# Optimization experiments

Measured on AMD Instinct MI355X. Metric: run time of the kernel, lower is better.

The kernel has to match this reference:

```python
import jax, jax.numpy as jnp
import numpy as np

N = 500000
V = 50000
GF = 64
OC = 256

def _lin(key, din, dout):
    k1, k2 = jax.random.split(key)
    w = jax.random.normal(k1, (din, dout), dtype=jnp.float32) * 0.02
    b = jax.random.normal(k2, (dout,), dtype=jnp.float32) * 0.02
    return w, b

def setup_inputs() -> dict:
    key = jax.random.key(0)
    ks = jax.random.split(key, 12)
    inp_feat = jax.random.normal(ks[0], (N, 6), dtype=jnp.float32)
    vox2point_idx = jax.random.randint(ks[1], (N,), 0, V, dtype=jnp.int32)
    w1x, b1x = _lin(ks[2], 3, GF)
    w2x, b2x = _lin(ks[3], GF, OC // 8)
    w1r, b1r = _lin(ks[4], 3, GF)
    w2r, b2r = _lin(ks[5], GF, OC // 8)
    wax, bax = _lin(ks[6], OC // 4, OC // 8)
    war, bar = _lin(ks[7], OC // 4, OC // 8)
    wv1, bv1 = _lin(ks[8], OC // 2, OC // 2)
    w3, b3 = _lin(ks[9], OC, OC)
    w4, b4 = _lin(ks[10], OC, OC)
    wv2, bv2 = _lin(ks[11], OC, OC)
    return dict(inp_feat=inp_feat, vox2point_idx=vox2point_idx, num_vox=V,
                w1x=w1x, b1x=b1x, w2x=w2x, b2x=b2x,
                w1r=w1r, b1r=b1r, w2r=w2r, b2r=b2r,
                wax=wax, bax=bax, war=war, bar=bar,
                wv1=wv1, bv1=bv1, w3=w3, b3=b3, w4=w4, b4=b4,
                wv2=wv2, bv2=bv2)

def reference(inp_feat, vox2point_idx, num_vox,
              w1x, b1x, w2x, b2x, w1r, b1r, w2r, b2r,
              wax, bax, war, bar, wv1, bv1, w3, b3, w4, b4, wv2, bv2):
    relu = jax.nn.relu
    xyz = inp_feat[:, :3]
    rgb = inp_feat[:, 3:]
    fx = relu(relu(xyz @ w1x + b1x) @ w2x + b2x)   # [N, 32]
    fr = relu(relu(rgb @ w1r + b1r) @ w2r + b2r)   # [N, 32]
    comb = jnp.concatenate([fx, fr], axis=-1)       # [N, 64]
    pf2 = jnp.concatenate([
        fx, fx * jax.nn.sigmoid(comb @ wax + bax),
        fr, fr * jax.nn.sigmoid(comb @ war + bar)], axis=-1)  # [N, 128]
    # scatter-max to voxels; torch_scatter fills empty segments with 0 and
    # pf2 >= 0 elementwise, so clamp -inf (jax empty fill) to 0 for parity.
    vox = jax.ops.segment_max(pf2, vox2point_idx, num_segments=num_vox)
    vox = jnp.maximum(vox, 0.0)                     # [V, 128]
    vox = relu(vox @ wv1 + bv1)
    pg = vox[vox2point_idx]                          # gather back [N, 128]
    pf3 = jnp.concatenate([pg, pf2], axis=-1)        # [N, 256]
    pf5 = relu(relu(pf3 @ w3 + b3) @ w4 + b4)        # [N, 256]
    vox2 = jax.ops.segment_max(pf5, vox2point_idx, num_segments=num_vox)
    vox2 = jnp.maximum(vox2, 0.0)
    return relu(vox2 @ wv2 + bv2)                    # [V, 256]
```

## Files before the change

kernel.cpp:

```cpp
#include <hip/hip_runtime.h>

#define NPTS 500000
#define NVOX 50000
#define NBLK 196

typedef unsigned short u16;
typedef unsigned int u32;
typedef __attribute__((ext_vector_type(8))) short short8;
typedef __attribute__((ext_vector_type(4))) float floatx4;
typedef __attribute__((ext_vector_type(4))) unsigned int uintx4;
typedef __attribute__((ext_vector_type(2))) unsigned int uintx2;

__device__ __forceinline__ u16 f2bf(float f) {
    u32 u = __float_as_uint(f);
    u = u + 0x7fffu + ((u >> 16) & 1u);
    return (u16)(u >> 16);
}

__global__ void k_wtransform(const float* __restrict__ W, u16* __restrict__ Wf, int K, int N) {
    int t = blockIdx.x * 256 + threadIdx.x;
    if (t >= K * N) return;
    int k = t / N, n = t - k * N;
    int kk = k >> 5, q = (k >> 3) & 3, j = k & 7;
    Wf[((size_t)((kk * 4 + q) * N + n) << 3) + j] = f2bf(W[t]);
}

__global__ void k_wcat(const float* __restrict__ w2x, const float* __restrict__ w2r, u16* __restrict__ wcatf) {
    int t = blockIdx.x * 256 + threadIdx.x;
    if (t >= 128 * 64) return;
    int k = t >> 6, n = t & 63;
    float v;
    if (k < 64) v = (n < 32) ? w2x[k * 32 + n] : 0.f;
    else        v = (n >= 32) ? w2r[(k - 64) * 32 + (n - 32)] : 0.f;
    int kk = k >> 5, q = (k >> 3) & 3, j = k & 7;
    wcatf[((size_t)((kk * 4 + q) * 64 + n) << 3) + j] = f2bf(v);
}

__global__ void k_watt(const float* __restrict__ wax, const float* __restrict__ war, u16* __restrict__ wattf) {
    int t = blockIdx.x * 256 + threadIdx.x;
    if (t >= 64 * 64) return;
    int k = t >> 6, n = t & 63;
    float v = (n < 32) ? wax[k * 32 + n] : war[k * 32 + (n - 32)];
    int kk = k >> 5, q = (k >> 3) & 3, j = k & 7;
    wattf[((size_t)((kk * 4 + q) * 64 + n) << 3) + j] = f2bf(v);
}

__global__ void k_hist(const int* __restrict__ idx, int* __restrict__ hcnt) {
    int i = blockIdx.x * 256 + threadIdx.x;
    if (i < NPTS) atomicAdd(&hcnt[idx[i]], 1);
}

__global__ __launch_bounds__(256) void k_scan1(const int* __restrict__ hcnt, int* __restrict__ bsum) {
    __shared__ int wsum[4];
    int t = threadIdx.x;
    int i = blockIdx.x * 256 + t;
    int c = (i < NVOX) ? hcnt[i] : 0;
    #pragma unroll
    for (int d = 32; d >= 1; d >>= 1) c += __shfl_xor(c, d, 64);
    if ((t & 63) == 0) wsum[t >> 6] = c;
    __syncthreads();
    if (t == 0) bsum[blockIdx.x] = wsum[0] + wsum[1] + wsum[2] + wsum[3];
}

__global__ __launch_bounds__(256) void k_scan2(const int* __restrict__ bsum, int* __restrict__ boff) {
    __shared__ int wsum[4];
    int t = threadIdx.x, lane = t & 63, w = t >> 6;
    int c = (t < NBLK) ? bsum[t] : 0;
    int v = c;
    #pragma unroll
    for (int d = 1; d < 64; d <<= 1) {
        int o = __shfl_up(v, d, 64);
        if (lane >= d) v += o;
    }
    if (lane == 63) wsum[w] = v;
    __syncthreads();
    int wo = 0;
    #pragma unroll
    for (int k = 0; k < 4; k++) if (k < w) wo += wsum[k];
    if (t < NBLK) boff[t] = wo + v - c;
}

__global__ __launch_bounds__(256) void k_scan3(const int* __restrict__ hcnt, const int* __restrict__ boff,
                                               int* __restrict__ cur) {
    __shared__ int wsum[4];
    int t = threadIdx.x, lane = t & 63, w = t >> 6;
    int i = blockIdx.x * 256 + t;
    int c = (i < NVOX) ? hcnt[i] : 0;
    int v = c;
    #pragma unroll
    for (int d = 1; d < 64; d <<= 1) {
        int o = __shfl_up(v, d, 64);
        if (lane >= d) v += o;
    }
    if (lane == 63) wsum[w] = v;
    __syncthreads();
    int wo = 0;
    #pragma unroll
    for (int k = 0; k < 4; k++) if (k < w) wo += wsum[k];
    if (i < NVOX) cur[i] = boff[blockIdx.x] + wo + v - c;
}

__global__ void k_scatter(const int* __restrict__ idx, int* __restrict__ cur,
                          int* __restrict__ sptid, int* __restrict__ svid) {
    int i = blockIdx.x * 256 + threadIdx.x;
    if (i < NPTS) {
        int v = idx[i];
        int pos = atomicAdd(&cur[v], 1);
        sptid[pos] = i;
        svid[pos] = v;
    }
}

__global__ __launch_bounds__(256) void k_pointfeat(
    const float* __restrict__ inp, const int* __restrict__ sptid, const int* __restrict__ svid,
    const float* __restrict__ w1x, const float* __restrict__ b1x,
    const float* __restrict__ w1r, const float* __restrict__ b1r,
    const u16* __restrict__ wcatf, const float* __restrict__ b2x, const float* __restrict__ b2r,
    const u16* __restrict__ wattf, const float* __restrict__ bax, const float* __restrict__ bar,
    u16* __restrict__ pf2s, float* __restrict__ voxmax)
{
    __shared__ u16 hbuf[64 * 136];
    __shared__ u16 cbuf[64 * 72];
    __shared__ float wl[512];
    __shared__ int lvid[64];
    int t = threadIdx.x;
    int i0 = blockIdx.x * 64;
    int mcnt = NPTS - i0; if (mcnt > 64) mcnt = 64;
    for (int s = t; s < 512; s += 256) {
        float v;
        if (s < 192)      v = w1x[s];
        else if (s < 256) v = b1x[s - 192];
        else if (s < 448) v = w1r[s - 256];
        else              v = b1r[s - 448];
        wl[s] = v;
    }
    if (t < 64) lvid[t] = (t < mcnt) ? svid[i0 + t] : -1;
    __syncthreads();
    {
        int m = t >> 2, c = t & 3;
        float x0 = 0, x1 = 0, x2 = 0, r0 = 0, r1 = 0, r2 = 0;
        if (m < mcnt) {
            const float* p = inp + (size_t)sptid[i0 + m] * 6;
            x0 = p[0]; x1 = p[1]; x2 = p[2]; r0 = p[3]; r1 = p[4]; r2 = p[5];
        }
        u16* hb = &hbuf[m * 136 + c * 16];
        #pragma unroll
        for (int jp = 0; jp < 8; jp++) {
            int c0 = c * 16 + 2 * jp, c1 = c0 + 1;
            float hx0 = fmaxf(wl[192 + c0] + x0 * wl[c0] + x1 * wl[64 + c0] + x2 * wl[128 + c0], 0.f);
            float hx1 = fmaxf(wl[192 + c1] + x0 * wl[c1] + x1 * wl[64 + c1] + x2 * wl[128 + c1], 0.f);
            float hr0 = fmaxf(wl[448 + c0] + r0 * wl[256 + c0] + r1 * wl[320 + c0] + r2 * wl[384 + c0], 0.f);
            float hr1 = fmaxf(wl[448 + c1] + r0 * wl[256 + c1] + r1 * wl[320 + c1] + r2 * wl[384 + c1], 0.f);
            *(u32*)(hb + 2 * jp)      = (u32)f2bf(hx0) | ((u32)f2bf(hx1) << 16);
            *(u32*)(hb + 64 + 2 * jp) = (u32)f2bf(hr0) | ((u32)f2bf(hr1) << 16);
        }
    }
    __syncthreads();
    int wave = t >> 6, l = t & 63, q = l >> 4, lm = l & 15;
    int n = wave * 16 + lm;
    floatx4 acc[4];
    #pragma unroll
    for (int a = 0; a < 4; a++) acc[a] = (floatx4){0.f, 0.f, 0.f, 0.f};
    #pragma unroll
    for (int kk = 0; kk < 4; kk++) {
        short8 bfrag = *(const short8*)&wcatf[(size_t)((kk * 4 + q) * 64 + n) << 3];
        #pragma unroll
        for (int tm = 0; tm < 4; tm++) {
            short8 afrag = *(const short8*)&hbuf[(tm * 16 + lm) * 136 + kk * 32 + q * 8];
            acc[tm] = __builtin_amdgcn_mfma_f32_16x16x32_bf16(afrag, bfrag, acc[tm], 0, 0, 0);
        }
    }
    float bv = (n < 32) ? b2x[n] : b2r[n - 32];
    float comb_keep[4][4];
    #pragma unroll
    for (int tm = 0; tm < 4; tm++)
        #pragma unroll
        for (int r = 0; r < 4; r++) {
            float v = fmaxf(acc[tm][r] + bv, 0.f);
            comb_keep[tm][r] = v;
            int m = tm * 16 + q * 4 + r;
            cbuf[m * 72 + n] = f2bf(v);
        }
    __syncthreads();
    floatx4 acc2[4];
    #pragma unroll
    for (int a = 0; a < 4; a++) acc2[a] = (floatx4){0.f, 0.f, 0.f, 0.f};
    #pragma unroll
    for (int kk = 0; kk < 2; kk++) {
        short8 bfrag = *(const short8*)&wattf[(size_t)((kk * 4 + q) * 64 + n) << 3];
        #pragma unroll
        for (int tm = 0; tm < 4; tm++) {
            short8 afrag = *(const short8*)&cbuf[(tm * 16 + lm) * 72 + kk * 32 + q * 8];
            acc2[tm] = __builtin_amdgcn_mfma_f32_16x16x32_bf16(afrag, bfrag, acc2[tm], 0, 0, 0);
        }
    }
    float bv2 = (n < 32) ? bax[n] : bar[n - 32];
    int pp = (n < 32) ? n : 32 + n;
    #pragma unroll
    for (int tm = 0; tm < 4; tm++)
        #pragma unroll
        for (int r = 0; r < 4; r++) {
            float att = acc2[tm][r] + bv2;
            float sg = 1.f / (1.f + __expf(-att));
            float plain = comb_keep[tm][r];
            float gated = plain * sg;
            int m = tm * 16 + q * 4 + r;
            hbuf[m * 136 + pp] = f2bf(plain);
            hbuf[m * 136 + pp + 32] = f2bf(gated);
        }
    __syncthreads();
    {
        int row = t >> 2, seg = t & 3;
        if (row < mcnt) {
            const u16* src = &hbuf[row * 136 + seg * 32];
            u16* dst = pf2s + (size_t)(i0 + row) * 128 + seg * 32;
            *(uintx4*)dst = *(const uintx4*)src;
            *(uintx4*)(dst + 8) = *(const uintx4*)(src + 8);
        }
    }
    {
        int c2 = t & 63;
        int h = t >> 6;
        int r0 = h * 16;
        int r1 = r0 + 16; if (r1 > mcnt) r1 = mcnt;
        u32 mlo = 0, mhi = 0;
        int pvid = -1;
        for (int r = r0; r < r1; r++) {
            int vid = lvid[r];
            if (vid != pvid) {
                if (pvid >= 0) {
                    int* addr = (int*)(voxmax + (size_t)pvid * 128 + 2 * c2);
                    if (mlo) atomicMax(addr, (int)(mlo << 16));
                    if (mhi) atomicMax(addr + 1, (int)(mhi << 16));
                }
                pvid = vid; mlo = 0; mhi = 0;
            }
            u32 u = *(const u32*)&hbuf[r * 136 + 2 * c2];
            u32 lo = u & 0xffffu, hi = u >> 16;
            mlo = lo > mlo ? lo : mlo;
            mhi = hi > mhi ? hi : mhi;
        }
        if (pvid >= 0) {
            int* addr = (int*)(voxmax + (size_t)pvid * 128 + 2 * c2);
            if (mlo) atomicMax(addr, (int)(mlo << 16));
            if (mhi) atomicMax(addr + 1, (int)(mhi << 16));
        }
    }
}

template<int K, int N, bool ABF16, bool OUT_BF16>
__global__ __launch_bounds__(256) void k_gemm_relu(
    const void* __restrict__ Ap, const u16* __restrict__ Wf,
    const float* __restrict__ bias, void* __restrict__ outp, int M)
{
    constexpr int STRIDE = K + 8;
    constexpr int TN = N / 64;
    constexpr int KSTEPS = K / 32;
    constexpr int CW = K / 4;
    __shared__ u16 lds[64 * STRIDE];
    int i0 = blockIdx.x * 64;
    int mcnt = M - i0; if (mcnt > 64) mcnt = 64;
    int t = threadIdx.x;
    {
        int row = t >> 2, cseg = t & 3;
        u16* dst = &lds[row * STRIDE + cseg * CW];
        if (row < mcnt) {
            if (ABF16) {
                const u16* src = (const u16*)Ap + (size_t)(i0 + row) * K + cseg * CW;
                #pragma unroll
                for (int c = 0; c < CW / 8; c++)
                    *(uintx4*)(dst + c * 8) = *(const uintx4*)(src + c * 8);
            } else {
                const float* src = (const float*)Ap + (size_t)(i0 + row) * K + cseg * CW;
                #pragma unroll
                for (int c = 0; c < CW / 8; c++) {
                    float4 v0 = *(const float4*)(src + c * 8);
                    float4 v1 = *(const float4*)(src + c * 8 + 4);
                    short8 rr;
                    rr[0] = f2bf(v0.x); rr[1] = f2bf(v0.y); rr[2] = f2bf(v0.z); rr[3] = f2bf(v0.w);
                    rr[4] = f2bf(v1.x); rr[5] = f2bf(v1.y); rr[6] = f2bf(v1.z); rr[7] = f2bf(v1.w);
                    *(short8*)(dst + c * 8) = rr;
                }
            }
        } else {
            short8 z = {0, 0, 0, 0, 0, 0, 0, 0};
            #pragma unroll
            for (int c = 0; c < CW / 8; c++) *(short8*)(dst + c * 8) = z;
        }
    }
    __syncthreads();
    int wave = t >> 6, l = t & 63;
    int q = l >> 4, lm = l & 15;
    int wn0 = wave * (N / 4);
    floatx4 acc[4][TN];
    #pragma unroll
    for (int a = 0; a < 4; a++)
        #pragma unroll
        for (int b = 0; b < TN; b++) acc[a][b] = (floatx4){0.f, 0.f, 0.f, 0.f};
    #pragma unroll
    for (int kk = 0; kk < KSTEPS; kk++) {
        short8 afrag[4], bfrag[TN];
        #pragma unroll
        for (int tm = 0; tm < 4; tm++)
            afrag[tm] = *(const short8*)&lds[(tm * 16 + lm) * STRIDE + kk * 32 + q * 8];
        #pragma unroll
        for (int tn = 0; tn < TN; tn++)
            bfrag[tn] = *(const short8*)&Wf[(size_t)((kk * 4 + q) * N + wn0 + tn * 16 + lm) * 8];
        #pragma unroll
        for (int tm = 0; tm < 4; tm++)
            #pragma unroll
            for (int tn = 0; tn < TN; tn++)
                acc[tm][tn] = __builtin_amdgcn_mfma_f32_16x16x32_bf16(afrag[tm], bfrag[tn], acc[tm][tn], 0, 0, 0);
    }
    #pragma unroll
    for (int tm = 0; tm < 4; tm++)
        #pragma unroll
        for (int tn = 0; tn < TN; tn++) {
            int n = wn0 + tn * 16 + lm;
            float bv = bias[n];
            #pragma unroll
            for (int r = 0; r < 4; r++) {
                int m = tm * 16 + q * 4 + r;
                if (m < mcnt) {
                    float v = fmaxf(acc[tm][tn][r] + bv, 0.f);
                    if (OUT_BF16) ((u16*)outp)[(size_t)(i0 + m) * N + n] = f2bf(v);
                    else          ((float*)outp)[(size_t)(i0 + m) * N + n] = v;
                }
            }
        }
}

__global__ __launch_bounds__(256) void k_pointmlp(
    const u16* __restrict__ voxf, const u16* __restrict__ pf2s, const int* __restrict__ svid,
    const u16* __restrict__ w3f, const float* __restrict__ b3,
    const u16* __restrict__ w4f, const float* __restrict__ b4,
    float* __restrict__ vox2)
{
    constexpr int STRIDE = 264;
    __shared__ u16 lds[64 * STRIDE];
    __shared__ int lvid[64];
    __shared__ float bl[512];
    int i0 = blockIdx.x * 64;
    int mcnt = NPTS - i0; if (mcnt > 64) mcnt = 64;
    int t = threadIdx.x;
    if (t < 64) lvid[t] = (t < mcnt) ? svid[i0 + t] : -1;
    for (int s = t; s < 512; s += 256) bl[s] = (s < 256) ? b3[s] : b4[s - 256];
    {
        int row = t >> 2, cseg = t & 3;
        u16* dst = &lds[row * STRIDE + cseg * 64];
        if (row < mcnt) {
            const u16* src;
            if (cseg < 2) src = voxf + (size_t)svid[i0 + row] * 128 + cseg * 64;
            else          src = pf2s + (size_t)(i0 + row) * 128 + (cseg - 2) * 64;
            #pragma unroll
            for (int c = 0; c < 8; c++)
                *(uintx4*)(dst + c * 8) = *(const uintx4*)(src + c * 8);
        } else {
            uintx4 z = {0, 0, 0, 0};
            #pragma unroll
            for (int c = 0; c < 8; c++) *(uintx4*)(dst + c * 8) = z;
        }
    }
    __syncthreads();
    int wave = t >> 6, l = t & 63;
    int q = l >> 4, lm = l & 15;
    int wm0 = wave * 64;
    floatx4 acc[4][4];
    #pragma unroll
    for (int a = 0; a < 4; a++)
        #pragma unroll
        for (int b = 0; b < 4; b++) acc[a][b] = (floatx4){0.f, 0.f, 0.f, 0.f};
    #pragma unroll
    for (int kk = 0; kk < 8; kk++) {
        short8 wfrag[4], bfrag[4];
        #pragma unroll
        for (int tm = 0; tm < 4; tm++)
            wfrag[tm] = *(const short8*)&w3f[(size_t)((kk * 4 + q) * 256 + wm0 + tm * 16 + lm) * 8];
        #pragma unroll
        for (int tn = 0; tn < 4; tn++)
            bfrag[tn] = *(const short8*)&lds[(tn * 16 + lm) * STRIDE + kk * 32 + q * 8];
        #pragma unroll
        for (int tm = 0; tm < 4; tm++)
            #pragma unroll
            for (int tn = 0; tn < 4; tn++)
                acc[tm][tn] = __builtin_amdgcn_mfma_f32_16x16x32_bf16(wfrag[tm], bfrag[tn], acc[tm][tn], 0, 0, 0);
    }
    __syncthreads();
    #pragma unroll
    for (int tm = 0; tm < 4; tm++) {
        float4 bq = *(const float4*)&bl[wm0 + tm * 16 + 4 * q];
        #pragma unroll
        for (int tn = 0; tn < 4; tn++) {
            u32 lo = (u32)f2bf(fmaxf(acc[tm][tn][0] + bq.x, 0.f)) | ((u32)f2bf(fmaxf(acc[tm][tn][1] + bq.y, 0.f)) << 16);
            u32 hi = (u32)f2bf(fmaxf(acc[tm][tn][2] + bq.z, 0.f)) | ((u32)f2bf(fmaxf(acc[tm][tn][3] + bq.w, 0.f)) << 16);
            *(uintx2*)&lds[(tn * 16 + lm) * STRIDE + wm0 + tm * 16 + 4 * q] = (uintx2){lo, hi};
        }
    }
    __syncthreads();
    floatx4 acc2[4][4];
    #pragma unroll
    for (int a = 0; a < 4; a++)
        #pragma unroll
        for (int b = 0; b < 4; b++) acc2[a][b] = (floatx4){0.f, 0.f, 0.f, 0.f};
    #pragma unroll
    for (int kk = 0; kk < 8; kk++) {
        short8 wfrag[4], bfrag[4];
        #pragma unroll
        for (int tm = 0; tm < 4; tm++)
            wfrag[tm] = *(const short8*)&w4f[(size_t)((kk * 4 + q) * 256 + wm0 + tm * 16 + lm) * 8];
        #pragma unroll
        for (int tn = 0; tn < 4; tn++)
            bfrag[tn] = *(const short8*)&lds[(tn * 16 + lm) * STRIDE + kk * 32 + q * 8];
        #pragma unroll
        for (int tm = 0; tm < 4; tm++)
            #pragma unroll
            for (int tn = 0; tn < 4; tn++)
                acc2[tm][tn] = __builtin_amdgcn_mfma_f32_16x16x32_bf16(wfrag[tm], bfrag[tn], acc2[tm][tn], 0, 0, 0);
    }
    __syncthreads();
    #pragma unroll
    for (int tm = 0; tm < 4; tm++) {
        float4 bq = *(const float4*)&bl[256 + wm0 + tm * 16 + 4 * q];
        #pragma unroll
        for (int tn = 0; tn < 4; tn++) {
            u32 lo = (u32)f2bf(fmaxf(acc2[tm][tn][0] + bq.x, 0.f)) | ((u32)f2bf(fmaxf(acc2[tm][tn][1] + bq.y, 0.f)) << 16);
            u32 hi = (u32)f2bf(fmaxf(acc2[tm][tn][2] + bq.z, 0.f)) | ((u32)f2bf(fmaxf(acc2[tm][tn][3] + bq.w, 0.f)) << 16);
            *(uintx2*)&lds[(tn * 16 + lm) * STRIDE + wm0 + tm * 16 + 4 * q] = (uintx2){lo, hi};
        }
    }
    __syncthreads();
    {
        int c2 = t & 127;
        int h = t >> 7;
        int r0 = h * 32;
        int r1 = r0 + 32; if (r1 > mcnt) r1 = mcnt;
        u32 mlo = 0, mhi = 0;
        int pvid = -1;
        for (int r = r0; r < r1; r++) {
            int vid = lvid[r];
            if (vid != pvid) {
                if (pvid >= 0) {
                    int* addr = (int*)(vox2 + (size_t)pvid * 256 + 2 * c2);
                    if (mlo) atomicMax(addr, (int)(mlo << 16));
                    if (mhi) atomicMax(addr + 1, (int)(mhi << 16));
                }
                pvid = vid; mlo = 0; mhi = 0;
            }
            u32 u = *(const u32*)&lds[r * STRIDE + 2 * c2];
            u32 lo = u & 0xffffu, hi = u >> 16;
            mlo = lo > mlo ? lo : mlo;
            mhi = hi > mhi ? hi : mhi;
        }
        if (pvid >= 0) {
            int* addr = (int*)(vox2 + (size_t)pvid * 256 + 2 * c2);
            if (mlo) atomicMax(addr, (int)(mlo << 16));
            if (mhi) atomicMax(addr + 1, (int)(mhi << 16));
        }
    }
}

extern "C" void kernel_launch(void* const* d_in, const int* in_sizes, int n_in,
                              void* d_out, int out_size, void* d_ws, size_t ws_size,
                              hipStream_t stream) {
    const float* inp = (const float*)d_in[0];
    const int*   idx = (const int*)d_in[1];
    const float* w1x = (const float*)d_in[3];  const float* b1x = (const float*)d_in[4];
    const float* w2x = (const float*)d_in[5];  const float* b2x = (const float*)d_in[6];
    const float* w1r = (const float*)d_in[7];  const float* b1r = (const float*)d_in[8];
    const float* w2r = (const float*)d_in[9];  const float* b2r = (const float*)d_in[10];
    const float* wax = (const float*)d_in[11]; const float* bax = (const float*)d_in[12];
    const float* war = (const float*)d_in[13]; const float* bar = (const float*)d_in[14];
    const float* wv1 = (const float*)d_in[15]; const float* bv1 = (const float*)d_in[16];
    const float* w3  = (const float*)d_in[17]; const float* b3  = (const float*)d_in[18];
    const float* w4  = (const float*)d_in[19]; const float* b4  = (const float*)d_in[20];
    const float* wv2 = (const float*)d_in[21]; const float* bv2 = (const float*)d_in[22];
    float* out = (float*)d_out;

    char* ws = (char*)d_ws;
    u16*   pf2s   = (u16*)ws;   ws += (size_t)NPTS * 128 * sizeof(u16);
    float* voxmax = (float*)ws; ws += (size_t)NVOX * 128 * sizeof(float);
    u16*   voxf   = (u16*)ws;   ws += (size_t)NVOX * 128 * sizeof(u16);
    float* vox2   = (float*)ws; ws += (size_t)NVOX * 256 * sizeof(float);
    u16*   w3f    = (u16*)ws;   ws += 65536 * sizeof(u16);
    u16*   w4f    = (u16*)ws;   ws += 65536 * sizeof(u16);
    u16*   wv1f   = (u16*)ws;   ws += 16384 * sizeof(u16);
    u16*   wv2f   = (u16*)ws;   ws += 65536 * sizeof(u16);
    u16*   wcatf  = (u16*)ws;   ws += 8192 * sizeof(u16);
    u16*   wattf  = (u16*)ws;   ws += 4096 * sizeof(u16);
    int*   hcnt   = (int*)ws;   ws += (size_t)NVOX * sizeof(int);
    int*   cur    = (int*)ws;   ws += (size_t)NVOX * sizeof(int);
    int*   bsum   = (int*)ws;   ws += (size_t)NBLK * sizeof(int);
    int*   boff   = (int*)ws;   ws += (size_t)NBLK * sizeof(int);
    int*   sptid  = (int*)ws;   ws += (size_t)NPTS * sizeof(int);
    int*   svid   = (int*)ws;   ws += (size_t)NPTS * sizeof(int);

    hipMemsetAsync(hcnt, 0, (size_t)NVOX * sizeof(int), stream);
    hipMemsetAsync(voxmax, 0, (size_t)NVOX * 128 * sizeof(float), stream);
    hipMemsetAsync(vox2, 0, (size_t)NVOX * 256 * sizeof(float), stream);

    k_wtransform<<<256, 256, 0, stream>>>(w3, w3f, 256, 256);
    k_wtransform<<<256, 256, 0, stream>>>(w4, w4f, 256, 256);
    k_wtransform<<<64,  256, 0, stream>>>(wv1, wv1f, 128, 128);
    k_wtransform<<<256, 256, 0, stream>>>(wv2, wv2f, 256, 256);
    k_wcat<<<32, 256, 0, stream>>>(w2x, w2r, wcatf);
    k_watt<<<16, 256, 0, stream>>>(wax, war, wattf);

    k_hist<<<(NPTS + 255) / 256, 256, 0, stream>>>(idx, hcnt);
    k_scan1<<<NBLK, 256, 0, stream>>>(hcnt, bsum);
    k_scan2<<<1, 256, 0, stream>>>(bsum, boff);
    k_scan3<<<NBLK, 256, 0, stream>>>(hcnt, boff, cur);
    k_scatter<<<(NPTS + 255) / 256, 256, 0, stream>>>(idx, cur, sptid, svid);

    k_pointfeat<<<(NPTS + 63) / 64, 256, 0, stream>>>(
        inp, sptid, svid, w1x, b1x, w1r, b1r, wcatf, b2x, b2r, wattf, bax, bar, pf2s, voxmax);

    k_gemm_relu<128, 128, false, true><<<(NVOX + 63) / 64, 256, 0, stream>>>(
        (const void*)voxmax, wv1f, bv1, (void*)voxf, NVOX);

    k_pointmlp<<<(NPTS + 63) / 64, 256, 0, stream>>>(
        voxf, pf2s, svid, w3f, b3, w4f, b4, vox2);

    k_gemm_relu<256, 256, false, false><<<(NVOX + 63) / 64, 256, 0, stream>>>(
        (const void*)vox2, wv2f, bv2, (void*)out, NVOX);
}
```

Baseline: 507.3 us.

## Swizzle pointmlp LDS, prefetch weights, use hardware bf16 pack and packed max

Replaces software bf16 rounding with the v_cvt_pk_bf16_f32 instruction and uses packed u16 max for the segment-max reductions. The pointmlp kernel drops its padded LDS stride for an XOR-swizzled 256-wide layout, which shrinks shared memory and raises the occupancy hint to 4 blocks per CU. It also double-buffers weight fragments across k-steps and reworks the final scatter so each thread handles 4 channels over 16 rows. Several independent micro-optimizations are combined, with some risk of register pressure under the new launch bound.

After: 696.4 us. +37.3%, slower.

```diff
diff --git a/kernel.cpp b/kernel.cpp
--- a/kernel.cpp
+++ b/kernel.cpp
@@ -10,11 +10,21 @@
 typedef __attribute__((ext_vector_type(4))) float floatx4;
 typedef __attribute__((ext_vector_type(4))) unsigned int uintx4;
 typedef __attribute__((ext_vector_type(2))) unsigned int uintx2;
-
+typedef __attribute__((ext_vector_type(2))) unsigned short us2;
+
+__device__ __forceinline__ u32 pkbf(float lo, float hi) {
+    u32 r;
+    asm("v_cvt_pk_bf16_f32 %0, %1, %2" : "=v"(r) : "v"(lo), "v"(hi));
+    return r;
+}
 __device__ __forceinline__ u16 f2bf(float f) {
-    u32 u = __float_as_uint(f);
-    u = u + 0x7fffu + ((u >> 16) & 1u);
-    return (u16)(u >> 16);
+    u32 r;
+    asm("v_cvt_pk_bf16_f32 %0, %1, %1" : "=v"(r) : "v"(f));
+    return (u16)r;
+}
+__device__ __forceinline__ u32 pmax(u32 a, u32 b) {
+    us2 r = __builtin_elementwise_max(__builtin_bit_cast(us2, a), __builtin_bit_cast(us2, b));
+    return __builtin_bit_cast(u32, r);
 }
 
 __global__ void k_wtransform(const float* __restrict__ W, u16* __restrict__ Wf, int K, int N) {
@@ -151,8 +161,8 @@
             float hx1 = fmaxf(wl[192 + c1] + x0 * wl[c1] + x1 * wl[64 + c1] + x2 * wl[128 + c1], 0.f);
             float hr0 = fmaxf(wl[448 + c0] + r0 * wl[256 + c0] + r1 * wl[320 + c0] + r2 * wl[384 + c0], 0.f);
             float hr1 = fmaxf(wl[448 + c1] + r0 * wl[256 + c1] + r1 * wl[320 + c1] + r2 * wl[384 + c1], 0.f);
-            *(u32*)(hb + 2 * jp)      = (u32)f2bf(hx0) | ((u32)f2bf(hx1) << 16);
-            *(u32*)(hb + 64 + 2 * jp) = (u32)f2bf(hr0) | ((u32)f2bf(hr1) << 16);
+            *(u32*)(hb + 2 * jp)      = pkbf(hx0, hx1);
+            *(u32*)(hb + 64 + 2 * jp) = pkbf(hr0, hr1);
         }
     }
     __syncthreads();
@@ -223,27 +233,25 @@
         int h = t >> 6;
         int r0 = h * 16;
         int r1 = r0 + 16; if (r1 > mcnt) r1 = mcnt;
-        u32 mlo = 0, mhi = 0;
+        u32 mm = 0;
         int pvid = -1;
         for (int r = r0; r < r1; r++) {
             int vid = lvid[r];
             if (vid != pvid) {
                 if (pvid >= 0) {
                     int* addr = (int*)(voxmax + (size_t)pvid * 128 + 2 * c2);
-                    if (mlo) atomicMax(addr, (int)(mlo << 16));
-                    if (mhi) atomicMax(addr + 1, (int)(mhi << 16));
+                    if (mm << 16) atomicMax(addr, (int)(mm << 16));
+                    if (mm & 0xffff0000u) atomicMax(addr + 1, (int)(mm & 0xffff0000u));
                 }
-                pvid = vid; mlo = 0; mhi = 0;
+                pvid = vid; mm = 0;
             }
             u32 u = *(const u32*)&hbuf[r * 136 + 2 * c2];
-            u32 lo = u & 0xffffu, hi = u >> 16;
-            mlo = lo > mlo ? lo : mlo;
-            mhi = hi > mhi ? hi : mhi;
+            mm = pmax(mm, u);
         }
         if (pvid >= 0) {
             int* addr = (int*)(voxmax + (size_t)pvid * 128 + 2 * c2);
-            if (mlo) atomicMax(addr, (int)(mlo << 16));
-            if (mhi) atomicMax(addr + 1, (int)(mhi << 16));
+            if (mm << 16) atomicMax(addr, (int)(mm << 16));
+            if (mm & 0xffff0000u) atomicMax(addr + 1, (int)(mm & 0xffff0000u));
         }
     }
 }
@@ -276,10 +284,9 @@
                 for (int c = 0; c < CW / 8; c++) {
                     float4 v0 = *(const float4*)(src + c * 8);
                     float4 v1 = *(const float4*)(src + c * 8 + 4);
-                    short8 rr;
-                    rr[0] = f2bf(v0.x); rr[1] = f2bf(v0.y); rr[2] = f2bf(v0.z); rr[3] = f2bf(v0.w);
-                    rr[4] = f2bf(v1.x); rr[5] = f2bf(v1.y); rr[6] = f2bf(v1.z); rr[7] = f2bf(v1.w);
-                    *(short8*)(dst + c * 8) = rr;
+                    uintx4 rr = (uintx4){ pkbf(v0.x, v0.y), pkbf(v0.z, v0.w),
+                                          pkbf(v1.x, v1.y), pkbf(v1.z, v1.w) };
+                    *(uintx4*)(dst + c * 8) = rr;
                 }
             }
         } else {
@@ -330,14 +337,13 @@
         }
 }
 
-__global__ __launch_bounds__(256) void k_pointmlp(
+__global__ __launch_bounds__(256, 4) void k_pointmlp(
     const u16* __restrict__ voxf, const u16* __restrict__ pf2s, const int* __restrict__ svid,
     const u16* __restrict__ w3f, const float* __restrict__ b3,
     const u16* __restrict__ w4f, const float* __restrict__ b4,
     float* __restrict__ vox2)
 {
-    constexpr int STRIDE = 264;
-    __shared__ u16 lds[64 * STRIDE];
+    __shared__ u16 lds[64 * 256];
     __shared__ int lvid[64];
     __shared__ float bl[512];
     int i0 = blockIdx.x * 64;
@@ -347,43 +353,61 @@
     for (int s = t; s < 512; s += 256) bl[s] = (s < 256) ? b3[s] : b4[s - 256];
     {
         int row = t >> 2, cseg = t & 3;
-        u16* dst = &lds[row * STRIDE + cseg * 64];
-        if (row < mcnt) {
-            const u16* src;
-            if (cseg < 2) src = voxf + (size_t)svid[i0 + row] * 128 + cseg * 64;
-            else          src = pf2s + (size_t)(i0 + row) * 128 + (cseg - 2) * 64;
-            #pragma unroll
-            for (int c = 0; c < 8; c++)
-                *(uintx4*)(dst + c * 8) = *(const uintx4*)(src + c * 8);
-        } else {
-            uintx4 z = {0, 0, 0, 0};
-            #pragma unroll
-            for (int c = 0; c < 8; c++) *(uintx4*)(dst + c * 8) = z;
+        const u16* srcb = nullptr;
+        if (row < mcnt)
+            srcb = (cseg < 2) ? voxf + (size_t)svid[i0 + row] * 128 + cseg * 64
+                              : pf2s + (size_t)(i0 + row) * 128 + (cseg - 2) * 64;
+        u16* dstb = &lds[row * 256 + cseg * 64];
+        int rx = row & 7;
+        #pragma unroll
+        for (int c = 0; c < 8; c++) {
+            int cc = (c + 2 * cseg) & 7;
+            uintx4 v = (uintx4){0, 0, 0, 0};
+            if (srcb) v = *(const uintx4*)(srcb + cc * 8);
+            *(uintx4*)(dstb + ((cc ^ rx) << 3)) = v;
         }
     }
     __syncthreads();
     int wave = t >> 6, l = t & 63;
     int q = l >> 4, lm = l & 15;
     int wm0 = wave * 64;
+    int lx = (lm & 7) << 4;
+    const char* ldsb = (const char*)lds;
+    char* ldsw = (char*)lds;
     floatx4 acc[4][4];
     #pragma unroll
     for (int a = 0; a < 4; a++)
         #pragma unroll
         for (int b = 0; b < 4; b++) acc[a][b] = (floatx4){0.f, 0.f, 0.f, 0.f};
-    #pragma unroll
-    for (int kk = 0; kk < 8; kk++) {
-        short8 wfrag[4], bfrag[4];
+    {
+        short8 wfrag[4];
         #pragma unroll
         for (int tm = 0; tm < 4; tm++)
-            wfrag[tm] = *(const short8*)&w3f[(size_t)((kk * 4 + q) * 256 + wm0 + tm * 16 + lm) * 8];
-        #pragma unroll
-        for (int tn = 0; tn < 4; tn++)
-            bfrag[tn] = *(const short8*)&lds[(tn * 16 + lm) * STRIDE + kk * 32 + q * 8];
-        #pragma unroll
-        for (int tm = 0; tm < 4; tm++)
-            #pragma unroll
-            for (int tn = 0; tn < 4; tn++)
-                acc[tm][tn] = __builtin_amdgcn_mfma_f32_16x16x32_bf16(wfrag[tm], bfrag[tn], acc[tm][tn], 0, 0, 0);
+            wfrag[tm] = *(const short8*)&w3f[(size_t)(q * 256 + wm0 + tm * 16 + lm) * 8];
+        #pragma unroll
+        for (int kk = 0; kk < 8; kk++) {
+            short8 wnext[4];
+            if (kk < 7) {
+                #pragma unroll
+                for (int tm = 0; tm < 4; tm++)
+                    wnext[tm] = *(const short8*)&w3f[(size_t)(((kk + 1) * 4 + q) * 256 + wm0 + tm * 16 + lm) * 8];
+            }
+            short8 bfrag[4];
+            #pragma unroll
+            for (int tn = 0; tn < 4; tn++) {
+                int ba = (((tn * 16 + lm) << 9) + (kk << 6) + (q << 4)) ^ lx;
+                bfrag[tn] = *(const short8*)(ldsb + ba);
+            }
+            #pragma unroll
+            for (int tm = 0; tm < 4; tm++)
+                #pragma unroll
+                for (int tn = 0; tn < 4; tn++)
+                    acc[tm][tn] = __builtin_amdgcn_mfma_f32_16x16x32_bf16(wfrag[tm], bfrag[tn], acc[tm][tn], 0, 0, 0);
+            if (kk < 7) {
+                #pragma unroll
+                for (int tm = 0; tm < 4; tm++) wfrag[tm] = wnext[tm];
+            }
+        }
     }
     __syncthreads();
     #pragma unroll
@@ -391,9 +415,10 @@
         float4 bq = *(const float4*)&bl[wm0 + tm * 16 + 4 * q];
         #pragma unroll
         for (int tn = 0; tn < 4; tn++) {
-            u32 lo = (u32)f2bf(fmaxf(acc[tm][tn][0] + bq.x, 0.f)) | ((u32)f2bf(fmaxf(acc[tm][tn][1] + bq.y, 0.f)) << 16);
-            u32 hi = (u32)f2bf(fmaxf(acc[tm][tn][2] + bq.z, 0.f)) | ((u32)f2bf(fmaxf(acc[tm][tn][3] + bq.w, 0.f)) << 16);
-            *(uintx2*)&lds[(tn * 16 + lm) * STRIDE + wm0 + tm * 16 + 4 * q] = (uintx2){lo, hi};
+            u32 lo = pkbf(fmaxf(acc[tm][tn][0] + bq.x, 0.f), fmaxf(acc[tm][tn][1] + bq.y, 0.f));
+            u32 hi = pkbf(fmaxf(acc[tm][tn][2] + bq.z, 0.f), fmaxf(acc[tm][tn][3] + bq.w, 0.f));
+            int ba = ((((tn * 16 + lm) << 9) + ((wm0 + tm * 16 + (q << 2)) << 1))) ^ lx;
+            *(uintx2*)(ldsw + ba) = (uintx2){lo, hi};
         }
     }
     __syncthreads();
@@ -402,20 +427,35 @@
     for (int a = 0; a < 4; a++)
         #pragma unroll
         for (int b = 0; b < 4; b++) acc2[a][b] = (floatx4){0.f, 0.f, 0.f, 0.f};
-    #pragma unroll
-    for (int kk = 0; kk < 8; kk++) {
-        short8 wfrag[4], bfrag[4];
+    {
+        short8 wfrag[4];
         #pragma unroll
         for (int tm = 0; tm < 4; tm++)
-            wfrag[tm] = *(const short8*)&w4f[(size_t)((kk * 4 + q) * 256 + wm0 + tm * 16 + lm) * 8];
-        #pragma unroll
-        for (int tn = 0; tn < 4; tn++)
-            bfrag[tn] = *(const short8*)&lds[(tn * 16 + lm) * STRIDE + kk * 32 + q * 8];
-        #pragma unroll
-        for (int tm = 0; tm < 4; tm++)
-            #pragma unroll
-            for (int tn = 0; tn < 4; tn++)
-                acc2[tm][tn] = __builtin_amdgcn_mfma_f32_16x16x32_bf16(wfrag[tm], bfrag[tn], acc2[tm][tn], 0, 0, 0);
+            wfrag[tm] = *(const short8*)&w4f[(size_t)(q * 256 + wm0 + tm * 16 + lm) * 8];
+        #pragma unroll
+        for (int kk = 0; kk < 8; kk++) {
+            short8 wnext[4];
+            if (kk < 7) {
+                #pragma unroll
+                for (int tm = 0; tm < 4; tm++)
+                    wnext[tm] = *(const short8*)&w4f[(size_t)(((kk + 1) * 4 + q) * 256 + wm0 + tm * 16 + lm) * 8];
+            }
+            short8 bfrag[4];
+            #pragma unroll
+            for (int tn = 0; tn < 4; tn++) {
+                int ba = (((tn * 16 + lm) << 9) + (kk << 6) + (q << 4)) ^ lx;
+                bfrag[tn] = *(const short8*)(ldsb + ba);
+            }
+            #pragma unroll
+            for (int tm = 0; tm < 4; tm++)
+                #pragma unroll
+                for (int tn = 0; tn < 4; tn++)
+                    acc2[tm][tn] = __builtin_amdgcn_mfma_f32_16x16x32_bf16(wfrag[tm], bfrag[tn], acc2[tm][tn], 0, 0, 0);
+            if (kk < 7) {
+                #pragma unroll
+                for (int tm = 0; tm < 4; tm++) wfrag[tm] = wnext[tm];
+            }
+        }
     }
     __syncthreads();
     #pragma unroll
@@ -423,38 +463,43 @@
         float4 bq = *(const float4*)&bl[256 + wm0 + tm * 16 + 4 * q];
         #pragma unroll
         for (int tn = 0; tn < 4; tn++) {
-            u32 lo = (u32)f2bf(fmaxf(acc2[tm][tn][0] + bq.x, 0.f)) | ((u32)f2bf(fmaxf(acc2[tm][tn][1] + bq.y, 0.f)) << 16);
-            u32 hi = (u32)f2bf(fmaxf(acc2[tm][tn][2] + bq.z, 0.f)) | ((u32)f2bf(fmaxf(acc2[tm][tn][3] + bq.w, 0.f)) << 16);
-            *(uintx2*)&lds[(tn * 16 + lm) * STRIDE + wm0 + tm * 16 + 4 * q] = (uintx2){lo, hi};
-        }
-    }
-    __syncthreads();
-    {
-        int c2 = t & 127;
-        int h = t >> 7;
-        int r0 = h * 32;
-        int r1 = r0 + 32; if (r1 > mcnt) r1 = mcnt;
-        u32 mlo = 0, mhi = 0;
+            u32 lo = pkbf(fmaxf(acc2[tm][tn][0] + bq.x, 0.f), fmaxf(acc2[tm][tn][1] + bq.y, 0.f));
+            u32 hi = pkbf(fmaxf(acc2[tm][tn][2] + bq.z, 0.f), fmaxf(acc2[tm][tn][3] + bq.w, 0.f));
+            int ba = ((((tn * 16 + lm) << 9) + ((wm0 + tm * 16 + (q << 2)) << 1))) ^ lx;
+            *(uintx2*)(ldsw + ba) = (uintx2){lo, hi};
+        }
+    }
+    __syncthreads();
+    {
+        int c4 = t & 63;
+        int h = t >> 6;
+        int r0 = h * 16;
+        int r1 = r0 + 16; if (r1 > mcnt) r1 = mcnt;
+        u32 m0 = 0, m1 = 0;
         int pvid = -1;
         for (int r = r0; r < r1; r++) {
             int vid = lvid[r];
             if (vid != pvid) {
                 if (pvid >= 0) {
-                    int* addr = (int*)(vox2 + (size_t)pvid * 256 + 2 * c2);
-                    if (mlo) atomicMax(addr, (int)(mlo << 16));
-                    if (mhi) atomicMax(addr + 1, (int)(mhi << 16));
+                    int* addr = (int*)(vox2 + (size_t)pvid * 256 + 4 * c4);
+                    if (m0 << 16) atomicMax(addr, (int)(m0 << 16));
+                    if (m0 & 0xffff0000u) atomicMax(addr + 1, (int)(m0 & 0xffff0000u));
+                    if (m1 << 16) atomicMax(addr + 2, (int)(m1 << 16));
+                    if (m1 & 0xffff0000u) atomicMax(addr + 3, (int)(m1 & 0xffff0000u));
                 }
-                pvid = vid; mlo = 0; mhi = 0;
-            }
-            u32 u = *(const u32*)&lds[r * STRIDE + 2 * c2];
-            u32 lo = u & 0xffffu, hi = u >> 16;
-            mlo = lo > mlo ? lo : mlo;
-            mhi = hi > mhi ? hi : mhi;
+                pvid = vid; m0 = 0; m1 = 0;
+            }
+            int ba = ((r << 9) + (c4 << 3)) ^ ((r & 7) << 4);
+            uintx2 u = *(const uintx2*)(ldsb + ba);
+            m0 = pmax(m0, u.x);
+            m1 = pmax(m1, u.y);
         }
         if (pvid >= 0) {
-            int* addr = (int*)(vox2 + (size_t)pvid * 256 + 2 * c2);
-            if (mlo) atomicMax(addr, (int)(mlo << 16));
-            if (mhi) atomicMax(addr + 1, (int)(mhi << 16));
+            int* addr = (int*)(vox2 + (size_t)pvid * 256 + 4 * c4);
+            if (m0 << 16) atomicMax(addr, (int)(m0 << 16));
+            if (m0 & 0xffff0000u) atomicMax(addr + 1, (int)(m0 & 0xffff0000u));
+            if (m1 << 16) atomicMax(addr + 2, (int)(m1 << 16));
+            if (m1 & 0xffff0000u) atomicMax(addr + 3, (int)(m1 & 0xffff0000u));
         }
     }
 }
```
